# Kernel tuning notes

Hardware: AMD Instinct MI355X
Metric: run time of the kernel (lower is better)

## Reference

```python
import jax, jax.numpy as jnp
import numpy as np

B, N = 16, 65536
N_BOUND = 50           # n_boundaries, linear spacing in [0, 1]
EMBD_LEN = N_BOUND + 1 # 51 learned bucket vectors
EMBD_DIM = 50
OUT_DIM = 50
HID = 2 * EMBD_DIM + 1 # 101, MLP width


def _xavier(key, shape):
    fan_in, fan_out = shape[1], shape[0]
    std = (2.0 / (fan_in + fan_out)) ** 0.5
    return jax.random.normal(key, shape, jnp.float32) * std


def setup_inputs() -> dict:
    key = jax.random.key(0)
    ks = jax.random.split(key, 6)
    x = jax.random.normal(ks[0], (B, N, 1), jnp.float32)
    boundaries = jnp.linspace(0.0, 1.0, N_BOUND).astype(jnp.float32)
    embd = _xavier(ks[1], (EMBD_LEN, EMBD_DIM))
    embd_oob = _xavier(ks[2], (2, OUT_DIM))
    w1 = _xavier(ks[3], (HID, HID))
    b1 = jnp.zeros((HID,), jnp.float32)
    w2 = _xavier(ks[4], (OUT_DIM, HID))
    b2 = jnp.zeros((OUT_DIM,), jnp.float32)
    return {"x": x, "boundaries": boundaries, "embd": embd,
            "embd_oob": embd_oob, "w1": w1, "b1": b1, "w2": w2, "b2": b2}


def reference(x, boundaries, embd, embd_oob, w1, b1, w2, b2):
    xv = x[..., 0]                                   # (B, N)
    # torch.searchsorted default (right=False) == jnp side='left'
    idx = jnp.searchsorted(boundaries, xv)           # in [0, N_BOUND]
    padded = jnp.concatenate([boundaries[:1], boundaries, boundaries[-1:]])  # (N_BOUND+2,)
    lo = padded[idx]
    hi = padded[idx + 1]
    rng = hi - lo
    # rng==0 only where idx is out-of-range (0 or EMBD_LEN-1); those outputs
    # are overwritten below, so guard the division to stay NaN-free.
    dist = (xv - lo) / jnp.where(rng == 0, 1.0, rng)  # (B, N)
    # in-range bucket indices live in [1, EMBD_LEN-2]; clip so idx+1 gather is safe
    ic = jnp.clip(idx, 1, EMBD_LEN - 2)
    feat = jnp.concatenate([embd[ic], embd[ic + 1], dist[..., None]], axis=-1)  # (B, N, 2*EMBD_DIM+1)
    h = jax.nn.gelu(feat @ w1.T + b1, approximate=False)  # torch nn.GELU = exact erf
    mlp_out = h @ w2.T + b2                           # (B, N, OUT_DIM)
    below = (idx == 0)[..., None]
    above = (idx == EMBD_LEN - 1)[..., None]
    out = jnp.where(below, embd_oob[0], jnp.where(above, embd_oob[1], mlp_out))
    return out
```

## Files before the change

### kernel.cpp

```cpp
#include <hip/hip_runtime.h>
#include <math.h>

#define NB        50
#define ED        50
#define OD        50
#define HID       101
#define K         129
#define NBUCKET   49
#define NSAMP     (NBUCKET * K)
#define NROWS     (NSAMP + 2)
#define ROWSTRIDE 52
#define NP        (16 * 65536)
#define CHUNK     17
#define NCHUNK    8

typedef float f32x2 __attribute__((ext_vector_type(2)));

__device__ __align__(16) float g_table[NROWS * ROWSTRIDE];

__global__ __launch_bounds__(256) void build_table(
    const float* __restrict__ embd,
    const float* __restrict__ embd_oob,
    const float* __restrict__ w1,
    const float* __restrict__ b1,
    const float* __restrict__ w2,
    const float* __restrict__ b2)
{
    const int blk = blockIdx.x;
    const int t   = threadIdx.x;

    if (blk == NBUCKET * NCHUNK) {
        if (t < 2 * OD) {
            const int which = t / OD, o = t - which * OD;
            g_table[(NSAMP + which) * ROWSTRIDE + o] = embd_oob[t];
        }
        return;
    }

    const int bu = blk >> 3;
    const int ch = blk & 7;

    __shared__ float w2s[OD * 104];
    __shared__ float hs[CHUNK * 104];
    __shared__ float zc[224];

    for (int i = t; i < OD * HID; i += 256) {
        const int o = i / HID, j = i - o * HID;
        w2s[o * 104 + j] = w2[i];
    }
    if (t < HID) {
        const float* __restrict__ w1r = w1 + t * HID;
        const float* __restrict__ ea  = embd + (bu + 1) * ED;
        float acc = b1[t];
        #pragma unroll 10
        for (int kk = 0; kk < ED; kk++)
            acc = fmaf(ea[kk], w1r[kk], fmaf(ea[ED + kk], w1r[ED + kk], acc));
        zc[t]       = acc;
        zc[112 + t] = w1r[2 * ED];
    }
    __syncthreads();

    #pragma unroll
    for (int si = 0; si < CHUNK; si++) {
        const int k = ch * CHUNK + si;
        if (t < HID && k < K) {
            const float dist = (float)k * (1.0f / 128.0f);
            const float z = fmaf(dist, zc[112 + t], zc[t]);
            hs[si * 104 + t] = 0.5f * z * (1.0f + erff(z * 0.70710678118654752f));
        }
    }
    __syncthreads();

    for (int d = t; d < CHUNK * OD; d += 256) {
        const int si = d / OD, o = d - si * OD;
        const int k = ch * CHUNK + si;
        if (k >= K) continue;
        float acc = b2[o];
        const float4* __restrict__ h4 = (const float4*)(hs  + si * 104);
        const float4* __restrict__ w4 = (const float4*)(w2s + o  * 104);
        #pragma unroll
        for (int jj = 0; jj < 25; jj++) {
            const float4 hh = h4[jj], ww = w4[jj];
            acc = fmaf(hh.x, ww.x, acc);
            acc = fmaf(hh.y, ww.y, acc);
            acc = fmaf(hh.z, ww.z, acc);
            acc = fmaf(hh.w, ww.w, acc);
        }
        acc = fmaf(hs[si * 104 + 100], w2s[o * 104 + 100], acc);
        g_table[(bu * K + k) * ROWSTRIDE + o] = acc;
    }
}

__global__ __launch_bounds__(256) void embed_main(
    const float* __restrict__ x,
    const float* __restrict__ boundaries,
    float* __restrict__ out)
{
    __shared__ float sB[NB];
    __shared__ int2  s_rows[256];
    __shared__ float s_frac[256];
    const int t = threadIdx.x;
    if (t < NB) sB[t] = boundaries[t];
    __syncthreads();

    const int p = blockIdx.x * 256 + t;
    const float xv = __builtin_nontemporal_load(&x[p]);

    int   row;
    float frac;
    if (xv <= sB[0]) {
        row = NSAMP;     frac = 0.0f;
    } else if (xv > sB[NB - 1]) {
        row = NSAMP + 1; frac = 0.0f;
    } else {
        int j = (int)(xv * 49.0f);
        if (j > 48) j = 48;
        const int idx = (xv > sB[j]) ? ((xv > sB[j + 1]) ? j + 2 : j + 1) : j;
        const float lo = sB[idx - 1];
        const float hi = sB[idx];
        const float dist = (xv - lo) / (hi - lo);
        const float tt = dist * 128.0f;
        int k0 = (int)tt;
        if (k0 > 127) k0 = 127;
        frac = tt - (float)k0;
        row  = (idx - 1) * K + k0;
    }
    const int row1 = row + (row < NSAMP ? 1 : 0);
    s_rows[t] = make_int2(row * 26, row1 * 26);
    s_frac[t] = frac;
    __syncthreads();

    const f32x2* __restrict__ tab = (const f32x2*)g_table;
    f32x2* __restrict__ o2 = (f32x2*)out + (size_t)blockIdx.x * 6400;

    #pragma unroll
    for (int i = 0; i < 25; i++) {
        const int e  = i * 256 + t;
        const int pt = e / 25;
        const int c2 = e - pt * 25;
        const int2  rr = s_rows[pt];
        const float fr = s_frac[pt];
        const f32x2 a = tab[rr.x + c2];
        const f32x2 b = tab[rr.y + c2];
        f32x2 r;
        r.x = fmaf(fr, b.x - a.x, a.x);
        r.y = fmaf(fr, b.y - a.y, a.y);
        __builtin_nontemporal_store(r, &o2[e]);
    }
}

extern "C" void kernel_launch(void* const* d_in, const int* in_sizes, int n_in,
                              void* d_out, int out_size, void* d_ws, size_t ws_size,
                              hipStream_t stream) {
    const float* x    = (const float*)d_in[0];
    const float* bnd  = (const float*)d_in[1];
    const float* embd = (const float*)d_in[2];
    const float* oob  = (const float*)d_in[3];
    const float* w1   = (const float*)d_in[4];
    const float* b1   = (const float*)d_in[5];
    const float* w2   = (const float*)d_in[6];
    const float* b2   = (const float*)d_in[7];
    float* out = (float*)d_out;

    build_table<<<NBUCKET * NCHUNK + 1, 256, 0, stream>>>(embd, oob, w1, b1, w2, b2);
    embed_main<<<NP / 256, 256, 0, stream>>>(x, bnd, out);
}
```

Measured before the change: 251.7 us.

## Store interpolation table in fp16 and serve out-of-range rows from shared memory

The precomputed per-bucket MLP output table is stored as half precision instead of float, which halves its footprint (about 6.3k rows of 52 entries) so more of it stays in cache during the gather-heavy main kernel. The two out-of-bounds embedding rows are moved out of the table into shared memory in the main kernel and selected with a negative row sentinel, which removes the extra build block. The cost is fp16 rounding of the table values, roughly 1e-3 relative error, plus a per-element branch in the output loop.

After: 246.0 us. 2.2% less time.

```diff
diff --git a/kernel.cpp b/kernel.cpp
--- a/kernel.cpp
+++ b/kernel.cpp
@@ -8,19 +8,18 @@
 #define K         129
 #define NBUCKET   49
 #define NSAMP     (NBUCKET * K)
-#define NROWS     (NSAMP + 2)
 #define ROWSTRIDE 52
 #define NP        (16 * 65536)
 #define CHUNK     17
 #define NCHUNK    8
 
-typedef float f32x2 __attribute__((ext_vector_type(2)));
+typedef float    f32x2 __attribute__((ext_vector_type(2)));
+typedef _Float16 f16x2 __attribute__((ext_vector_type(2)));
 
-__device__ __align__(16) float g_table[NROWS * ROWSTRIDE];
+__device__ __align__(16) _Float16 g_table[NSAMP * ROWSTRIDE];
 
 __global__ __launch_bounds__(256) void build_table(
     const float* __restrict__ embd,
-    const float* __restrict__ embd_oob,
     const float* __restrict__ w1,
     const float* __restrict__ b1,
     const float* __restrict__ w2,
@@ -28,17 +27,8 @@
 {
     const int blk = blockIdx.x;
     const int t   = threadIdx.x;
-
-    if (blk == NBUCKET * NCHUNK) {
-        if (t < 2 * OD) {
-            const int which = t / OD, o = t - which * OD;
-            g_table[(NSAMP + which) * ROWSTRIDE + o] = embd_oob[t];
-        }
-        return;
-    }
-
-    const int bu = blk >> 3;
-    const int ch = blk & 7;
+    const int bu  = blk >> 3;
+    const int ch  = blk & 7;
 
     __shared__ float w2s[OD * 104];
     __shared__ float hs[CHUNK * 104];
@@ -87,31 +77,34 @@
             acc = fmaf(hh.w, ww.w, acc);
         }
         acc = fmaf(hs[si * 104 + 100], w2s[o * 104 + 100], acc);
-        g_table[(bu * K + k) * ROWSTRIDE + o] = acc;
+        g_table[(bu * K + k) * ROWSTRIDE + o] = (_Float16)acc;
     }
 }
 
 __global__ __launch_bounds__(256) void embed_main(
     const float* __restrict__ x,
     const float* __restrict__ boundaries,
+    const float* __restrict__ embd_oob,
     float* __restrict__ out)
 {
     __shared__ float sB[NB];
+    __shared__ f32x2 sTail[50];
     __shared__ int2  s_rows[256];
     __shared__ float s_frac[256];
     const int t = threadIdx.x;
     if (t < NB) sB[t] = boundaries[t];
+    if (t < 2 * OD) ((float*)sTail)[t] = embd_oob[t];
     __syncthreads();
 
     const int p = blockIdx.x * 256 + t;
     const float xv = __builtin_nontemporal_load(&x[p]);
 
-    int   row;
-    float frac;
+    int   r0, r1;
+    float frac = 0.0f;
     if (xv <= sB[0]) {
-        row = NSAMP;     frac = 0.0f;
+        r0 = -1;  r1 = -1;
     } else if (xv > sB[NB - 1]) {
-        row = NSAMP + 1; frac = 0.0f;
+        r0 = -26; r1 = -26;
     } else {
         int j = (int)(xv * 49.0f);
         if (j > 48) j = 48;
@@ -123,14 +116,14 @@
         int k0 = (int)tt;
         if (k0 > 127) k0 = 127;
         frac = tt - (float)k0;
-        row  = (idx - 1) * K + k0;
+        const int row = (idx - 1) * K + k0;
+        r0 = row * 26; r1 = r0 + 26;
     }
-    const int row1 = row + (row < NSAMP ? 1 : 0);
-    s_rows[t] = make_int2(row * 26, row1 * 26);
+    s_rows[t] = make_int2(r0, r1);
     s_frac[t] = frac;
     __syncthreads();
 
-    const f32x2* __restrict__ tab = (const f32x2*)g_table;
+    const f16x2* __restrict__ tabh = (const f16x2*)g_table;
     f32x2* __restrict__ o2 = (f32x2*)out + (size_t)blockIdx.x * 6400;
 
     #pragma unroll
@@ -139,12 +132,17 @@
         const int pt = e / 25;
         const int c2 = e - pt * 25;
         const int2  rr = s_rows[pt];
-        const float fr = s_frac[pt];
-        const f32x2 a = tab[rr.x + c2];
-        const f32x2 b = tab[rr.y + c2];
         f32x2 r;
-        r.x = fmaf(fr, b.x - a.x, a.x);
-        r.y = fmaf(fr, b.y - a.y, a.y);
+        if (rr.x >= 0) {
+            const float fr = s_frac[pt];
+            const f16x2 a = tabh[rr.x + c2];
+            const f16x2 b = tabh[rr.y + c2];
+            const float ax = (float)a.x, ay = (float)a.y;
+            r.x = fmaf(fr, (float)b.x - ax, ax);
+            r.y = fmaf(fr, (float)b.y - ay, ay);
+        } else {
+            r = sTail[c2 - rr.x - 1];
+        }
         __builtin_nontemporal_store(r, &o2[e]);
     }
 }
@@ -162,6 +160,6 @@
     const float* b2   = (const float*)d_in[7];
     float* out = (float*)d_out;
 
-    build_table<<<NBUCKET * NCHUNK + 1, 256, 0, stream>>>(embd, oob, w1, b1, w2, b2);
-    embed_main<<<NP / 256, 256, 0, stream>>>(x, bnd, out);
+    build_table<<<NBUCKET * NCHUNK, 256, 0, stream>>>(embd, w1, b1, w2, b2);
+    embed_main<<<NP / 256, 256, 0, stream>>>(x, bnd, oob, out);
 }
```
